# Kernel tuning notes

Hardware: AMD Instinct MI355X
Metric: run time of the kernel (lower is better)

## Reference

```python
import jax, jax.numpy as jnp
import numpy as np

D_MODEL = 1024
N_HEADS = 16
D_HEAD = D_MODEL // N_HEADS


def setup_inputs() -> dict:
    key = jax.random.key(0)
    kx, kq, kk, kv = jax.random.split(key, 4)
    B, T = 2, 2048
    X = jax.random.normal(kx, (B, T, D_MODEL), dtype=jnp.float32)
    s = 1.0 / np.sqrt(D_MODEL)
    # torch nn.Linear weight is [out, in]; y = x @ W.T
    Wq = jax.random.uniform(kq, (D_MODEL, D_MODEL), jnp.float32, -s, s)
    Wk = jax.random.uniform(kk, (D_MODEL, D_MODEL), jnp.float32, -s, s)
    Wv = jax.random.uniform(kv, (D_MODEL, D_MODEL), jnp.float32, -s, s)
    return {"X": X, "Wq": Wq, "Wk": Wk, "Wv": Wv}


def reference(X, Wq, Wk, Wv):
    B, T, _ = X.shape
    def heads(W):
        # x @ W.T -> [B,T,D] -> [B,H,T,Dh]
        return (X @ W.T).reshape(B, T, N_HEADS, D_HEAD).transpose(0, 2, 1, 3)
    Q, K, V = heads(Wq), heads(Wk), heads(Wv)
    scores = jnp.einsum('bhqd,bhkd->bhqk', Q, K)
    causal = jnp.tril(jnp.ones((T, T), dtype=bool))
    # original masks with -inf BEFORE scaling; -inf/scale == -inf, so equivalent
    scores = jnp.where(causal, scores, -jnp.inf) / jnp.sqrt(jnp.float32(D_HEAD))
    attn = jax.nn.softmax(scores, axis=-1)
    out = jnp.einsum('bhqk,bhkd->bhqd', attn, V)
    return out.transpose(0, 2, 1, 3).reshape(B, T, N_HEADS * D_HEAD)
```

## Files before the change

### kernel.cpp

```cpp
#include <hip/hip_runtime.h>


using bf16x8   = __attribute__((ext_vector_type(8))) __bf16;
using floatx4  = __attribute__((ext_vector_type(4))) float;
using floatx16 = __attribute__((ext_vector_type(16))) float;
using uintx4   = __attribute__((ext_vector_type(4))) unsigned int;

#define T_SEQ   2048
#define D_MODEL 1024
#define N_HEADS 16
#define D_HEAD  64
#define BATCH   2
#define M_TOT   4096
#define N_TOT   3072
#define PLANE   (T_SEQ * D_HEAD)
#define NX      (M_TOT * D_MODEL)
#define NWSEG   (D_MODEL * D_MODEL)
#define QSCALE  0.18033688f
#define SM_BIAS 24.0f

__device__ __forceinline__ unsigned short f32_to_bf16(float f) {
  unsigned int u = __float_as_uint(f);
  u += 0x7fffu + ((u >> 16) & 1u);
  return (unsigned short)(u >> 16);
}
__device__ __forceinline__ unsigned int pack2_bf16(float a, float b) {
  unsigned int ua = __float_as_uint(a) + 0x8000u;
  unsigned int ub = __float_as_uint(b) + 0x8000u;
  return __builtin_amdgcn_perm(ub, ua, 0x07060302);
}
__device__ __forceinline__ void async_cp16(void* lds, const void* gptr) {
  __builtin_amdgcn_global_load_lds(
      (const __attribute__((address_space(1))) unsigned int*)gptr,
      (__attribute__((address_space(3))) unsigned int*)lds, 16, 0, 0);
}

__global__ __launch_bounds__(256) void cvt_kernel(
    const float* __restrict__ X,  const float* __restrict__ Wq,
    const float* __restrict__ Wk, const float* __restrict__ Wv,
    unsigned short* __restrict__ Xb, unsigned short* __restrict__ Wb)
{
  const size_t i = ((size_t)blockIdx.x * 256 + threadIdx.x) * 8;
  const float* src;
  unsigned short* dst;
  if (i < NX) { src = X + i; dst = Xb + i; }
  else {
    const size_t r = i - NX;
    const int w = (int)(r >> 20);
    const size_t o = r & (NWSEG - 1);
    src = ((w == 0) ? Wq : (w == 1) ? Wk : Wv) + o;
    dst = Wb + r;
  }
  float4 f0 = *(const float4*)src;
  float4 f1 = *(const float4*)(src + 4);
  uint4 out;
  out.x = pack2_bf16(f0.x, f0.y);
  out.y = pack2_bf16(f0.z, f0.w);
  out.z = pack2_bf16(f1.x, f1.y);
  out.w = pack2_bf16(f1.z, f1.w);
  *(uint4*)dst = out;
}

__global__ __launch_bounds__(512, 6) void gemm_qkv(
    const unsigned short* __restrict__ Xb,
    const unsigned short* __restrict__ Wb,
    unsigned short* __restrict__ Qb,
    unsigned short* __restrict__ Kb,
    unsigned short* __restrict__ VTb)
{
  __shared__ unsigned short Als[128 * 64];
  __shared__ unsigned short Bls[128 * 64];

  const int tid  = threadIdx.x;
  const int lane = tid & 63;
  const int wave = tid >> 6;
  const int l15  = lane & 15;
  const int quad = lane >> 4;
  const int wm   = wave & 3;
  const int wn   = wave >> 2;

  const int n_blk = blockIdx.x * 128;
  const int m_blk = blockIdx.y * 128;

  const int swz = (((tid >> 3) ^ tid) & 7) * 8;
  const unsigned short* Ag = Xb + (size_t)(m_blk + (tid >> 3)) * D_MODEL + swz;
  const unsigned short* Bg = Wb + (size_t)(n_blk + (tid >> 3)) * D_MODEL + swz;
  char* Alds = (char*)Als + wave * 1024;
  char* Blds = (char*)Bls + wave * 1024;

  floatx4 acc[2][4] = {};

  for (int k0 = 0; k0 < D_MODEL; k0 += 64) {
    __syncthreads();
#pragma unroll
    for (int p = 0; p < 2; p++) {
      async_cp16(Alds + p * 8192, Ag + (size_t)(p * 64) * D_MODEL + k0);
      async_cp16(Blds + p * 8192, Bg + (size_t)(p * 64) * D_MODEL + k0);
    }
    __syncthreads();

#pragma unroll
    for (int ks = 0; ks < 2; ks++) {
      bf16x8 a[2], b[4];
      const int sa = ((ks * 4 + quad) ^ (l15 & 7)) * 16;
#pragma unroll
      for (int i = 0; i < 2; i++)
        a[i] = *(const bf16x8*)((char*)Als + (wm * 32 + 16 * i + l15) * 128 + sa);
#pragma unroll
      for (int j = 0; j < 4; j++)
        b[j] = *(const bf16x8*)((char*)Bls + (wn * 64 + 16 * j + l15) * 128 + sa);
#pragma unroll
      for (int mi = 0; mi < 2; mi++)
#pragma unroll
        for (int ni = 0; ni < 4; ni++)
          acc[mi][ni] = __builtin_amdgcn_mfma_f32_16x16x32_bf16(a[mi], b[ni], acc[mi][ni], 0, 0, 0);
    }
  }

  __syncthreads();
  char* ep = (char*)Als + wave * 4096;
  const int w_sel  = n_blk >> 10;
  const int m_base = m_blk + wm * 32;
  const int n_base = n_blk + wn * 64;
  const int h      = (n_base & 1023) >> 6;
  const float csc  = (w_sel == 0) ? QSCALE : 1.0f;
  const int bb     = m_base >> 11;

  if (w_sel < 2) {
#pragma unroll
    for (int mi = 0; mi < 2; mi++)
#pragma unroll
      for (int ni = 0; ni < 4; ni++)
#pragma unroll
        for (int r = 0; r < 4; r++) {
          const int row  = 16 * mi + quad * 4 + r;
          const int colb = (16 * ni + l15) * 2;
          const int phys = ((colb >> 4) ^ (row & 7)) * 16;
          *(unsigned short*)(ep + row * 128 + phys + (colb & 15)) =
              f32_to_bf16(acc[mi][ni][r] * csc);
        }
  } else {
#pragma unroll
    for (int mi = 0; mi < 2; mi++)
#pragma unroll
      for (int ni = 0; ni < 4; ni++)
#pragma unroll
        for (int r = 0; r < 4; r++) {
          const int row  = 16 * ni + l15;
          const int colb = (16 * mi + quad * 4 + r) * 2;
          const int phys = ((colb >> 4) ^ (row & 3)) * 16;
          *(unsigned short*)(ep + row * 64 + phys + (colb & 15)) =
              f32_to_bf16(acc[mi][ni][r]);
        }
  }
  asm volatile("s_waitcnt lgkmcnt(0)" ::: "memory");

  if (w_sel < 2) {
#pragma unroll
    for (int pass = 0; pass < 4; pass++) {
      const int row = pass * 8 + (lane >> 3);
      const int cl  = (lane & 7) ^ (row & 7);
      uint4 v = *(const uint4*)(ep + row * 128 + (lane & 7) * 16);
      const int m = m_base + row;
      const int t = m & (T_SEQ - 1);
      unsigned short* dst = ((w_sel == 0) ? Qb : Kb) +
          ((size_t)(bb * N_HEADS + h) * T_SEQ + t) * D_HEAD + cl * 8;
      *(uint4*)dst = v;
    }
  } else {
#pragma unroll
    for (int pass = 0; pass < 4; pass++) {
      const int row = pass * 16 + (lane >> 2);
      const int cl  = (lane & 3) ^ (row & 3);
      uint4 v = *(const uint4*)(ep + row * 64 + (lane & 3) * 16);
      unsigned short* dst = VTb +
          ((size_t)(bb * N_HEADS + h) * D_HEAD + row) * T_SEQ +
          (m_base & (T_SEQ - 1)) + cl * 8;
      *(uint4*)dst = v;
    }
  }
}

__global__ __launch_bounds__(512, 4) void attn_kernel(
    const unsigned short* __restrict__ Qb,
    const unsigned short* __restrict__ Kb,
    const unsigned short* __restrict__ VTb,
    float* __restrict__ Out)
{
  __shared__ __align__(16) char smem[65536];

  const int tid  = threadIdx.x;
  const int lane = tid & 63;
  const int wave = tid >> 6;
  const int l31  = lane & 31;
  const int q1   = lane >> 5;
  const int wq   = wave & 1;
  const int wk   = (wave >> 1) & 1;
  const int wu   = wave >> 2;

  const int bh   = blockIdx.x & 31;
  const int pair = blockIdx.x >> 5;

  const unsigned short* Qp = Qb  + (size_t)bh * PLANE;
  const unsigned short* Kp = Kb  + (size_t)bh * PLANE;
  const unsigned short* Vp = VTb + (size_t)bh * PLANE;
  const int b = bh >> 4, h = bh & 15;

  const int rg = tid >> 3;
  const int sl = (tid ^ rg) & 7;
  const unsigned short* Kg = Kp + (size_t)rg * D_HEAD + sl * 8;
  const unsigned short* Vg = Vp + (size_t)rg * T_SEQ + sl * 8;

  float* const LB = (float*)(smem + 33792);

#define STAGE_CHUNK(c)                                                        \
  do {                                                                        \
    char* kd = smem + (((c) >> 1) & 1) * 16384 + ((c) & 1) * 8192             \
               + wave * 1024;                                                 \
    char* vd = smem + 32768 + (((c) >> 1) & 1) * 16384 + ((c) & 1) * 8192     \
               + wave * 1024;                                                 \
    async_cp16(kd, Kg + (size_t)(c) * (64 * D_HEAD));                         \
    async_cp16(vd, Vg + (size_t)(c) * 64);                                    \
  } while (0)

#pragma unroll 1
  for (int it = 0; it < 2; it++) {
    const int strip = it ? (31 - pair) : pair;
    const int qbase = strip * 64 + wq * 32;
    const int nch   = strip + 1;
    const int nm    = (nch + 1) >> 1;

    bf16x8 aq[4];
#pragma unroll
    for (int kp = 0; kp < 4; kp++)
      aq[kp] = *(const bf16x8*)(Qp + (size_t)(qbase + l31) * D_HEAD + kp * 16 + q1 * 8);

    floatx16 o0 = {}, o1 = {};
    float l_acc = 0.0f;

    __syncthreads();

    STAGE_CHUNK(0);
    STAGE_CHUNK(1);

#pragma unroll 1
    for (int m = 0; m < nm; m++) {
      if (m + 1 < nm) {
        STAGE_CHUNK(2 * m + 2);
        STAGE_CHUNK(2 * m + 3);
        asm volatile("s_waitcnt vmcnt(4)" ::: "memory");
      } else {
        asm volatile("s_waitcnt vmcnt(0)" ::: "memory");
      }
      __builtin_amdgcn_s_barrier();
      __builtin_amdgcn_sched_barrier(0);

      const int jc = 2 * m + wu;
      const int kbase = jc * 64 + wk * 32;

      if (jc < nch && kbase <= qbase + 31) {
        const char* Ksb = smem + ((jc >> 1) & 1) * 16384 + (jc & 1) * 8192;
        const char* Vsb = smem + 32768 + ((jc >> 1) & 1) * 16384 + (jc & 1) * 8192;

        floatx16 s = {};
        const int krow = wk * 32 + l31;
        __builtin_amdgcn_s_setprio(1);
#pragma unroll
        for (int kp = 0; kp < 4; kp++) {
          const int c = 2 * kp + q1;
          bf16x8 ak = *(const bf16x8*)(Ksb + krow * 128 + ((c ^ (krow & 7)) * 16));
          s = __builtin_amdgcn_mfma_f32_32x32x16_bf16(ak, aq[kp], s, 0, 0, 0);
        }
        __builtin_amdgcn_s_setprio(0);

        if (kbase >= qbase) {
          const int q = qbase + l31;
#pragma unroll
          for (int r = 0; r < 16; r++) {
            const int kk = kbase + (r & 3) + 8 * (r >> 2) + 4 * q1;
            if (kk > q) s[r] = -INFINITY;
          }
        }

        float pv[16];
#pragma unroll
        for (int r = 0; r < 16; r++)
          pv[r] = __builtin_amdgcn_exp2f(s[r] - SM_BIAS);
#pragma unroll
        for (int r = 0; r < 16; r += 4)
          l_acc += (pv[r] + pv[r + 1]) + (pv[r + 2] + pv[r + 3]);

        unsigned int w[8];
#pragma unroll
        for (int m2 = 0; m2 < 8; m2++)
          asm("v_cvt_pk_bf16_f32 %0, %1, %2" : "=v"(w[m2]) : "v"(pv[2 * m2]), "v"(pv[2 * m2 + 1]));

        __builtin_amdgcn_s_setprio(1);
#pragma unroll
        for (int kp = 0; kp < 2; kp++) {
          unsigned int b0 = w[4 * kp],     b2 = w[4 * kp + 2];
          unsigned int b1 = w[4 * kp + 1], b3 = w[4 * kp + 3];
          asm("v_permlane32_swap_b32 %0, %1" : "+v"(b0), "+v"(b2));
          asm("v_permlane32_swap_b32 %0, %1" : "+v"(b1), "+v"(b3));
          uintx4 uu; uu[0] = b0; uu[1] = b1; uu[2] = b2; uu[3] = b3;
          const bf16x8 pf = __builtin_bit_cast(bf16x8, uu);

          const int cv = 4 * wk + 2 * kp + q1;
          bf16x8 av0 = *(const bf16x8*)(Vsb + l31 * 128 + ((cv ^ (l31 & 7)) * 16));
          o0 = __builtin_amdgcn_mfma_f32_32x32x16_bf16(av0, pf, o0, 0, 0, 0);
          const int row1 = 32 + l31;
          bf16x8 av1 = *(const bf16x8*)(Vsb + row1 * 128 + ((cv ^ (row1 & 7)) * 16));
          o1 = __builtin_amdgcn_mfma_f32_32x32x16_bf16(av1, pf, o1, 0, 0, 0);
        }
        __builtin_amdgcn_s_setprio(0);
      }

      __builtin_amdgcn_sched_barrier(0);
      __builtin_amdgcn_s_barrier();
    }

    float la = l_acc, lb2 = l_acc;
    asm("v_permlane32_swap_b32 %0, %1" : "+v"(la), "+v"(lb2));
    const float lt = la + lb2;

    __syncthreads();

    float* ob = (float*)smem + (wk * 2 + wq) * (64 * 33);
    if (wu == 0) {
#pragma unroll
      for (int r = 0; r < 16; r++) {
        const int d0 = (r & 3) + 8 * (r >> 2) + 4 * q1;
        ob[d0 * 33 + l31]        = o0[r];
        ob[(32 + d0) * 33 + l31] = o1[r];
      }
    }
    if (lane < 32) LB[wave * 32 + l31] = lt;
    __syncthreads();
    if (wu == 1) {
#pragma unroll
      for (int r = 0; r < 16; r++) {
        const int d0 = (r & 3) + 8 * (r >> 2) + 4 * q1;
        ob[d0 * 33 + l31]        += o0[r];
        ob[(32 + d0) * 33 + l31] += o1[r];
      }
    }
    __syncthreads();

    const int row = tid >> 3;
    const int dg  = tid & 7;
    const int wqr = row >> 5, ql = row & 31;
    const float lsum = (LB[wqr * 32 + ql]       + LB[(wqr + 2) * 32 + ql]) +
                       (LB[(wqr + 4) * 32 + ql] + LB[(wqr + 6) * 32 + ql]);
    const float inv = 1.0f / lsum;
    const float* p0 = (const float*)smem + (0 * 2 + wqr) * (64 * 33);
    const float* p1 = (const float*)smem + (1 * 2 + wqr) * (64 * 33);

    float vout[8];
#pragma unroll
    for (int i = 0; i < 8; i++) {
      const int d = dg * 8 + i;
      vout[i] = (p0[d * 33 + ql] + p1[d * 33 + ql]) * inv;
    }
    const int t = strip * 64 + row;
    float* dst = Out + (size_t)(b * T_SEQ + t) * D_MODEL + h * D_HEAD + dg * 8;
    *(float4*)(dst)     = *(const float4*)(vout);
    *(float4*)(dst + 4) = *(const float4*)(vout + 4);
  }
#undef STAGE_CHUNK
}

extern "C" void kernel_launch(void* const* d_in, const int* in_sizes, int n_in,
                              void* d_out, int out_size, void* d_ws, size_t ws_size,
                              hipStream_t stream) {
  const float* X  = (const float*)d_in[0];
  const float* Wq = (const float*)d_in[1];
  const float* Wk = (const float*)d_in[2];
  const float* Wv = (const float*)d_in[3];

  unsigned short* Qb = (unsigned short*)d_ws;
  unsigned short* Kb = Qb + (size_t)BATCH * N_HEADS * T_SEQ * D_HEAD;
  unsigned short* VT = Kb + (size_t)BATCH * N_HEADS * T_SEQ * D_HEAD;

  unsigned short* Xb = (unsigned short*)d_out;
  unsigned short* Wb = Xb + (size_t)NX;

  cvt_kernel<<<3584, 256, 0, stream>>>(X, Wq, Wk, Wv, Xb, Wb);

  dim3 g1(N_TOT / 128, M_TOT / 128);
  gemm_qkv<<<g1, 512, 0, stream>>>(Xb, Wb, Qb, Kb, VT);

  attn_kernel<<<512, 512, 0, stream>>>(Qb, Kb, VT, (float*)d_out);
}
```

Before: 136.0 us.

## Double-buffer LDS tiles in QKV GEMM to overlap async loads with MFMA

The QKV projection GEMM now keeps two LDS buffers for the A and B tiles and issues the async global-to-LDS copy for the next k-tile before computing the current one. A partial vmcnt wait and raw s_barrier replace the two __syncthreads per iteration, so global load latency can be hidden behind MFMA work. LDS use doubles and launch bounds drop from 6 to 4 blocks per CU, which lowers occupancy in exchange for the overlap.

```diff
diff --git a/kernel.cpp b/kernel.cpp
--- a/kernel.cpp
+++ b/kernel.cpp
@@ -61,15 +61,15 @@
   *(uint4*)dst = out;
 }
 
-__global__ __launch_bounds__(512, 6) void gemm_qkv(
+__global__ __launch_bounds__(512, 4) void gemm_qkv(
     const unsigned short* __restrict__ Xb,
     const unsigned short* __restrict__ Wb,
     unsigned short* __restrict__ Qb,
     unsigned short* __restrict__ Kb,
     unsigned short* __restrict__ VTb)
 {
-  __shared__ unsigned short Als[128 * 64];
-  __shared__ unsigned short Bls[128 * 64];
+  __shared__ unsigned short Als[2][128 * 64];
+  __shared__ unsigned short Bls[2][128 * 64];
 
   const int tid  = threadIdx.x;
   const int lane = tid & 63;
@@ -85,37 +85,56 @@
   const int swz = (((tid >> 3) ^ tid) & 7) * 8;
   const unsigned short* Ag = Xb + (size_t)(m_blk + (tid >> 3)) * D_MODEL + swz;
   const unsigned short* Bg = Wb + (size_t)(n_blk + (tid >> 3)) * D_MODEL + swz;
-  char* Alds = (char*)Als + wave * 1024;
-  char* Blds = (char*)Bls + wave * 1024;
 
   floatx4 acc[2][4] = {};
 
-  for (int k0 = 0; k0 < D_MODEL; k0 += 64) {
-    __syncthreads();
-#pragma unroll
-    for (int p = 0; p < 2; p++) {
-      async_cp16(Alds + p * 8192, Ag + (size_t)(p * 64) * D_MODEL + k0);
-      async_cp16(Blds + p * 8192, Bg + (size_t)(p * 64) * D_MODEL + k0);
-    }
-    __syncthreads();
-
+#define STAGE_G(kt)                                                           \
+  do {                                                                        \
+    char* ad = (char*)Als[(kt) & 1] + wave * 1024;                            \
+    char* bd = (char*)Bls[(kt) & 1] + wave * 1024;                            \
+    _Pragma("unroll")                                                         \
+    for (int p = 0; p < 2; p++) {                                             \
+      async_cp16(ad + p * 8192, Ag + (size_t)(p * 64) * D_MODEL + (kt) * 64); \
+      async_cp16(bd + p * 8192, Bg + (size_t)(p * 64) * D_MODEL + (kt) * 64); \
+    }                                                                         \
+  } while (0)
+
+  STAGE_G(0);
+
+#pragma unroll 1
+  for (int kt = 0; kt < 16; kt++) {
+    if (kt + 1 < 16) {
+      STAGE_G(kt + 1);
+      asm volatile("s_waitcnt vmcnt(4)" ::: "memory");
+    } else {
+      asm volatile("s_waitcnt vmcnt(0)" ::: "memory");
+    }
+    __builtin_amdgcn_s_barrier();
+    __builtin_amdgcn_sched_barrier(0);
+
+    const char* Ab = (const char*)Als[kt & 1];
+    const char* Bb = (const char*)Bls[kt & 1];
 #pragma unroll
     for (int ks = 0; ks < 2; ks++) {
       bf16x8 a[2], b[4];
       const int sa = ((ks * 4 + quad) ^ (l15 & 7)) * 16;
 #pragma unroll
       for (int i = 0; i < 2; i++)
-        a[i] = *(const bf16x8*)((char*)Als + (wm * 32 + 16 * i + l15) * 128 + sa);
+        a[i] = *(const bf16x8*)(Ab + (wm * 32 + 16 * i + l15) * 128 + sa);
 #pragma unroll
       for (int j = 0; j < 4; j++)
-        b[j] = *(const bf16x8*)((char*)Bls + (wn * 64 + 16 * j + l15) * 128 + sa);
+        b[j] = *(const bf16x8*)(Bb + (wn * 64 + 16 * j + l15) * 128 + sa);
 #pragma unroll
       for (int mi = 0; mi < 2; mi++)
 #pragma unroll
         for (int ni = 0; ni < 4; ni++)
           acc[mi][ni] = __builtin_amdgcn_mfma_f32_16x16x32_bf16(a[mi], b[ni], acc[mi][ni], 0, 0, 0);
     }
+
+    __builtin_amdgcn_sched_barrier(0);
+    __builtin_amdgcn_s_barrier();
   }
+#undef STAGE_G
 
   __syncthreads();
   char* ep = (char*)Als + wave * 4096;
```

After: 144.2 us. +6.0%, slower.
